# Performance work log

Hardware: AMD Instinct MI355X
Metric: run time of the kernel (lower is better)

## Reference

```python
import jax, jax.numpy as jnp
import numpy as np

# ---- static problem configuration (mirrors Barrier_Net param) ----
B, NN, NO, SD = 100000, 16, 8, 4        # agents, neighbors, obstacles, state dim
H, PHI_OUT, ADIM = 64, 16, 2            # MLP hidden, deepset latent, action dim
DS, B_GAMMA, B_EXPH = 0.2, 0.01, 1.0    # r_safe, barrier gain, barrier exponent
PHI_MIN, PHI_MAX = -1.0, 1.0            # empty-action range
A_MIN, A_MAX = -2.0, 2.0                # final action range
D_OBS = 1 + (NN + 1) * SD + 2 * NO      # 85


def mlp2(x, w1, b1, w2, b2):
    return jax.nn.relu(x @ w1 + b1) @ w2 + b2


def setup_inputs() -> dict:
    key = jax.random.key(0)
    ks = jax.random.split(key, 10)
    x = jax.random.normal(ks[0], (B, D_OBS), jnp.float32)
    x = x.at[:, 0].set(float(NN))  # first entry encodes the neighbor count

    def w(k, shape):
        return jax.random.normal(k, shape, jnp.float32) * 0.1

    return {
        "x": x,
        "phi_w1": w(ks[1], (SD, H)), "phi_b1": jnp.zeros((H,), jnp.float32),
        "phi_w2": w(ks[2], (H, PHI_OUT)), "phi_b2": jnp.zeros((PHI_OUT,), jnp.float32),
        "obs_w1": w(ks[3], (2, H)), "obs_b1": jnp.zeros((H,), jnp.float32),
        "obs_w2": w(ks[4], (H, PHI_OUT)), "obs_b2": jnp.zeros((PHI_OUT,), jnp.float32),
        "rho_w1": w(ks[5], (PHI_OUT, H)), "rho_b1": jnp.zeros((H,), jnp.float32),
        "rho_w2": w(ks[6], (H, ADIM)), "rho_b2": jnp.zeros((ADIM,), jnp.float32),
        "psi_w1": w(ks[7], (ADIM + 2, H)), "psi_b1": jnp.zeros((H,), jnp.float32),
        "psi_w2": w(ks[8], (H, ADIM)), "psi_b2": jnp.zeros((ADIM,), jnp.float32),
    }


def reference(x, phi_w1, phi_b1, phi_w2, phi_b2, obs_w1, obs_b1, obs_w2, obs_b2,
              rho_w1, rho_b1, rho_w2, rho_b2, psi_w1, psi_b1, psi_w2, psi_b2):
    # observation layout: [nn, self(SD), nn relative neighbor states(SD each), no obstacles(2 each)]
    nb = x[:, 1 + SD:1 + SD + NN * SD].reshape(B, NN, SD)   # relative neighbor states
    ob = x[:, 1 + (NN + 1) * SD:].reshape(B, NO, 2)          # relative obstacle positions

    # --- DeepSet: permutation-invariant sum of phi over elements, then rho ---
    phi_sum = mlp2(nb, phi_w1, phi_b1, phi_w2, phi_b2).sum(axis=1)   # [B, PHI_OUT]
    obs_sum = mlp2(ob, obs_w1, obs_b1, obs_w2, obs_b2).sum(axis=1)   # [B, PHI_OUT]
    rho = mlp2(phi_sum + obs_sum, rho_w1, rho_b1, rho_w2, rho_b2)    # [B, ADIM]

    # --- empty(): psi head on cat(rho, g) with tanh range squash to [phi_min, phi_max] ---
    g = x[:, 0:2]
    e = mlp2(jnp.concatenate([rho, g], axis=1), psi_w1, psi_b1, psi_w2, psi_b2)
    empty = (jnp.tanh(e) + 1.0) * 0.5 * (PHI_MAX - PHI_MIN) + PHI_MIN

    # --- barrier: gather neighbor rel-positions, scalar potential, scatter-add per agent ---
    p_ij = -nb[..., 0:2]                                    # [B, NN, 2], p^i - p^j
    h_ij = jnp.linalg.norm(p_ij, axis=-1) - DS              # [B, NN]
    barrier = jnp.sum((B_GAMMA / h_ij ** B_EXPH)[..., None] * p_ij, axis=1)  # [B, 2]

    action = jnp.tanh(empty + barrier)
    return (action + 1.0) * 0.5 * (A_MAX - A_MIN) + A_MIN
```

## Files before the change

kernel.cpp:

```cpp
#include <hip/hip_runtime.h>

#define BATCH 100000

__device__ __forceinline__ float relu(float v) { return fmaxf(v, 0.f); }

__global__ __launch_bounds__(256, 4) void barrier_net(
    const float* __restrict__ x,
    const float* __restrict__ phi_w1, const float* __restrict__ phi_b1,
    const float* __restrict__ phi_w2, const float* __restrict__ phi_b2,
    const float* __restrict__ obs_w1, const float* __restrict__ obs_b1,
    const float* __restrict__ obs_w2, const float* __restrict__ obs_b2,
    const float* __restrict__ rho_w1, const float* __restrict__ rho_b1,
    const float* __restrict__ rho_w2, const float* __restrict__ rho_b2,
    const float* __restrict__ psi_w1, const float* __restrict__ psi_b1,
    const float* __restrict__ psi_w2, const float* __restrict__ psi_b2,
    float2* __restrict__ out)
{
    const int s = blockIdx.x * 256 + threadIdx.x;
    if (s >= BATCH) return;
    const float* xr = x + (size_t)s * 85;

    float g0 = xr[0];
    float g1 = xr[1];
    float nb[16][4];
#pragma unroll
    for (int n = 0; n < 16; ++n)
#pragma unroll
        for (int k = 0; k < 4; ++k)
            nb[n][k] = xr[5 + n * 4 + k];

    float bar0 = 0.f, bar1 = 0.f;
#pragma unroll
    for (int n = 0; n < 16; ++n) {
        float p0 = -nb[n][0], p1 = -nb[n][1];
        float r  = __builtin_amdgcn_sqrtf(fmaf(p0, p0, p1 * p1));
        float sc = 0.01f * __builtin_amdgcn_rcpf(r - 0.2f);
        bar0 = fmaf(sc, p0, bar0);
        bar1 = fmaf(sc, p1, bar1);
    }

    float acc[16];
#pragma unroll
    for (int j = 0; j < 16; ++j)
        acc[j] = fmaf(16.f, phi_b2[j], 8.f * obs_b2[j]);

#pragma unroll 2
    for (int h = 0; h < 64; ++h) {
        float w0 = phi_w1[h], w1 = phi_w1[64 + h], w2 = phi_w1[128 + h], w3 = phi_w1[192 + h];
        float b  = phi_b1[h];
        float hs = 0.f;
#pragma unroll
        for (int n = 0; n < 16; ++n) {
            float t = fmaf(nb[n][0], w0, fmaf(nb[n][1], w1, fmaf(nb[n][2], w2, fmaf(nb[n][3], w3, b))));
            hs += relu(t);
        }
#pragma unroll
        for (int j = 0; j < 16; ++j)
            acc[j] = fmaf(hs, phi_w2[h * 16 + j], acc[j]);
    }

    float obv[8][2];
#pragma unroll
    for (int o = 0; o < 8; ++o) {
        obv[o][0] = xr[69 + o * 2];
        obv[o][1] = xr[69 + o * 2 + 1];
    }
#pragma unroll 2
    for (int h = 0; h < 64; ++h) {
        float w0 = obs_w1[h], w1 = obs_w1[64 + h];
        float b  = obs_b1[h];
        float hs = 0.f;
#pragma unroll
        for (int o = 0; o < 8; ++o)
            hs += relu(fmaf(obv[o][0], w0, fmaf(obv[o][1], w1, b)));
#pragma unroll
        for (int j = 0; j < 16; ++j)
            acc[j] = fmaf(hs, obs_w2[h * 16 + j], acc[j]);
    }

    float r0 = rho_b2[0], r1 = rho_b2[1];
#pragma unroll 2
    for (int h = 0; h < 64; ++h) {
        float t = rho_b1[h];
#pragma unroll
        for (int j = 0; j < 16; ++j)
            t = fmaf(acc[j], rho_w1[j * 64 + h], t);
        t = relu(t);
        r0 = fmaf(t, rho_w2[2 * h],     r0);
        r1 = fmaf(t, rho_w2[2 * h + 1], r1);
    }

    float e0 = psi_b2[0], e1 = psi_b2[1];
#pragma unroll 2
    for (int h = 0; h < 64; ++h) {
        float t = fmaf(r0, psi_w1[h],
                  fmaf(r1, psi_w1[64 + h],
                  fmaf(g0, psi_w1[128 + h],
                  fmaf(g1, psi_w1[192 + h], psi_b1[h]))));
        t = relu(t);
        e0 = fmaf(t, psi_w2[2 * h],     e0);
        e1 = fmaf(t, psi_w2[2 * h + 1], e1);
    }

    float a0 = tanhf(tanhf(e0) + bar0);
    float a1 = tanhf(tanhf(e1) + bar1);
    out[s] = make_float2(2.f * a0, 2.f * a1);
}

extern "C" void kernel_launch(void* const* d_in, const int* in_sizes, int n_in,
                              void* d_out, int out_size, void* d_ws, size_t ws_size,
                              hipStream_t stream) {
    dim3 grid((BATCH + 255) / 256), block(256);
    barrier_net<<<grid, block, 0, stream>>>(
        (const float*)d_in[0],
        (const float*)d_in[1],  (const float*)d_in[2],  (const float*)d_in[3],  (const float*)d_in[4],
        (const float*)d_in[5],  (const float*)d_in[6],  (const float*)d_in[7],  (const float*)d_in[8],
        (const float*)d_in[9],  (const float*)d_in[10], (const float*)d_in[11], (const float*)d_in[12],
        (const float*)d_in[13], (const float*)d_in[14], (const float*)d_in[15], (const float*)d_in[16],
        (float2*)d_out);
}
```

Measured before the change: 154.2 us.

## Split each agent across four lanes with shuffle reductions

Each agent is now handled by four consecutive threads. Each lane processes 4 neighbors and 2 obstacles and a quarter of the rho and psi hidden units, and partial sums are combined with xor shuffles. This raises parallelism and cuts the per-thread register footprint, which allows higher occupancy (launch bounds raised to 8). In exchange it adds shuffle overhead, and every lane still recomputes the full 16-wide phi and obs output accumulation from its partial hidden sums.

```diff
diff --git a/kernel.cpp b/kernel.cpp
--- a/kernel.cpp
+++ b/kernel.cpp
@@ -4,7 +4,7 @@
 
 __device__ __forceinline__ float relu(float v) { return fmaxf(v, 0.f); }
 
-__global__ __launch_bounds__(256, 4) void barrier_net(
+__global__ __launch_bounds__(256, 8) void barrier_net(
     const float* __restrict__ x,
     const float* __restrict__ phi_w1, const float* __restrict__ phi_b1,
     const float* __restrict__ phi_w2, const float* __restrict__ phi_b2,
@@ -16,22 +16,30 @@
     const float* __restrict__ psi_w2, const float* __restrict__ psi_b2,
     float2* __restrict__ out)
 {
-    const int s = blockIdx.x * 256 + threadIdx.x;
+    const int tid = blockIdx.x * 256 + threadIdx.x;
+    const int s = tid >> 2;
+    const int t = tid & 3;
     if (s >= BATCH) return;
     const float* xr = x + (size_t)s * 85;
 
-    float g0 = xr[0];
-    float g1 = xr[1];
-    float nb[16][4];
+    float nb[4][4];
+    const int nbase = 5 + 16 * t;
 #pragma unroll
-    for (int n = 0; n < 16; ++n)
+    for (int n = 0; n < 4; ++n)
 #pragma unroll
         for (int k = 0; k < 4; ++k)
-            nb[n][k] = xr[5 + n * 4 + k];
+            nb[n][k] = xr[nbase + 4 * n + k];
+
+    float ob[2][2];
+    const int obase = 69 + 4 * t;
+    ob[0][0] = xr[obase];     ob[0][1] = xr[obase + 1];
+    ob[1][0] = xr[obase + 2]; ob[1][1] = xr[obase + 3];
+
+    const float g0 = xr[0], g1 = xr[1];
 
     float bar0 = 0.f, bar1 = 0.f;
 #pragma unroll
-    for (int n = 0; n < 16; ++n) {
+    for (int n = 0; n < 4; ++n) {
         float p0 = -nb[n][0], p1 = -nb[n][1];
         float r  = __builtin_amdgcn_sqrtf(fmaf(p0, p0, p1 * p1));
         float sc = 0.01f * __builtin_amdgcn_rcpf(r - 0.2f);
@@ -42,75 +50,94 @@
     float acc[16];
 #pragma unroll
     for (int j = 0; j < 16; ++j)
-        acc[j] = fmaf(16.f, phi_b2[j], 8.f * obs_b2[j]);
+        acc[j] = fmaf(4.f, phi_b2[j], 2.f * obs_b2[j]);
 
-#pragma unroll 2
+#pragma unroll 4
     for (int h = 0; h < 64; ++h) {
         float w0 = phi_w1[h], w1 = phi_w1[64 + h], w2 = phi_w1[128 + h], w3 = phi_w1[192 + h];
         float b  = phi_b1[h];
-        float hs = 0.f;
-#pragma unroll
-        for (int n = 0; n < 16; ++n) {
-            float t = fmaf(nb[n][0], w0, fmaf(nb[n][1], w1, fmaf(nb[n][2], w2, fmaf(nb[n][3], w3, b))));
-            hs += relu(t);
-        }
+        float hs = relu(fmaf(nb[0][0], w0, fmaf(nb[0][1], w1, fmaf(nb[0][2], w2, fmaf(nb[0][3], w3, b)))))
+                 + relu(fmaf(nb[1][0], w0, fmaf(nb[1][1], w1, fmaf(nb[1][2], w2, fmaf(nb[1][3], w3, b)))))
+                 + relu(fmaf(nb[2][0], w0, fmaf(nb[2][1], w1, fmaf(nb[2][2], w2, fmaf(nb[2][3], w3, b)))))
+                 + relu(fmaf(nb[3][0], w0, fmaf(nb[3][1], w1, fmaf(nb[3][2], w2, fmaf(nb[3][3], w3, b)))));
 #pragma unroll
         for (int j = 0; j < 16; ++j)
             acc[j] = fmaf(hs, phi_w2[h * 16 + j], acc[j]);
     }
 
-    float obv[8][2];
-#pragma unroll
-    for (int o = 0; o < 8; ++o) {
-        obv[o][0] = xr[69 + o * 2];
-        obv[o][1] = xr[69 + o * 2 + 1];
-    }
-#pragma unroll 2
+#pragma unroll 4
     for (int h = 0; h < 64; ++h) {
         float w0 = obs_w1[h], w1 = obs_w1[64 + h];
         float b  = obs_b1[h];
-        float hs = 0.f;
-#pragma unroll
-        for (int o = 0; o < 8; ++o)
-            hs += relu(fmaf(obv[o][0], w0, fmaf(obv[o][1], w1, b)));
+        float hs = relu(fmaf(ob[0][0], w0, fmaf(ob[0][1], w1, b)))
+                 + relu(fmaf(ob[1][0], w0, fmaf(ob[1][1], w1, b)));
 #pragma unroll
         for (int j = 0; j < 16; ++j)
             acc[j] = fmaf(hs, obs_w2[h * 16 + j], acc[j]);
     }
 
-    float r0 = rho_b2[0], r1 = rho_b2[1];
+#pragma unroll
+    for (int j = 0; j < 16; ++j) {
+        acc[j] += __shfl_xor(acc[j], 1);
+        acc[j] += __shfl_xor(acc[j], 2);
+    }
+    bar0 += __shfl_xor(bar0, 1); bar0 += __shfl_xor(bar0, 2);
+    bar1 += __shfl_xor(bar1, 1); bar1 += __shfl_xor(bar1, 2);
+
+    float r0 = 0.f, r1 = 0.f;
+    {
+        const float* rw1 = rho_w1 + 16 * t;
+        const float* rw2 = rho_w2 + 32 * t;
+        const float* rb1 = rho_b1 + 16 * t;
 #pragma unroll 2
-    for (int h = 0; h < 64; ++h) {
-        float t = rho_b1[h];
+        for (int i = 0; i < 16; ++i) {
+            float tt = rb1[i];
 #pragma unroll
-        for (int j = 0; j < 16; ++j)
-            t = fmaf(acc[j], rho_w1[j * 64 + h], t);
-        t = relu(t);
-        r0 = fmaf(t, rho_w2[2 * h],     r0);
-        r1 = fmaf(t, rho_w2[2 * h + 1], r1);
+            for (int j = 0; j < 16; ++j)
+                tt = fmaf(acc[j], rw1[j * 64 + i], tt);
+            tt = relu(tt);
+            r0 = fmaf(tt, rw2[2 * i],     r0);
+            r1 = fmaf(tt, rw2[2 * i + 1], r1);
+        }
     }
+    r0 += __shfl_xor(r0, 1); r0 += __shfl_xor(r0, 2);
+    r1 += __shfl_xor(r1, 1); r1 += __shfl_xor(r1, 2);
+    r0 += rho_b2[0];
+    r1 += rho_b2[1];
 
-    float e0 = psi_b2[0], e1 = psi_b2[1];
+    float e0 = 0.f, e1 = 0.f;
+    {
+        const float* pw1 = psi_w1 + 16 * t;
+        const float* pw2 = psi_w2 + 32 * t;
+        const float* pb1 = psi_b1 + 16 * t;
 #pragma unroll 2
-    for (int h = 0; h < 64; ++h) {
-        float t = fmaf(r0, psi_w1[h],
-                  fmaf(r1, psi_w1[64 + h],
-                  fmaf(g0, psi_w1[128 + h],
-                  fmaf(g1, psi_w1[192 + h], psi_b1[h]))));
-        t = relu(t);
-        e0 = fmaf(t, psi_w2[2 * h],     e0);
-        e1 = fmaf(t, psi_w2[2 * h + 1], e1);
+        for (int i = 0; i < 16; ++i) {
+            float tt = fmaf(r0, pw1[i],
+                       fmaf(r1, pw1[64 + i],
+                       fmaf(g0, pw1[128 + i],
+                       fmaf(g1, pw1[192 + i], pb1[i]))));
+            tt = relu(tt);
+            e0 = fmaf(tt, pw2[2 * i],     e0);
+            e1 = fmaf(tt, pw2[2 * i + 1], e1);
+        }
     }
+    e0 += __shfl_xor(e0, 1); e0 += __shfl_xor(e0, 2);
+    e1 += __shfl_xor(e1, 1); e1 += __shfl_xor(e1, 2);
+    e0 += psi_b2[0];
+    e1 += psi_b2[1];
 
-    float a0 = tanhf(tanhf(e0) + bar0);
-    float a1 = tanhf(tanhf(e1) + bar1);
-    out[s] = make_float2(2.f * a0, 2.f * a1);
+    if (t == 0) {
+        float a0 = tanhf(tanhf(e0) + bar0);
+        float a1 = tanhf(tanhf(e1) + bar1);
+        out[s] = make_float2(2.f * a0, 2.f * a1);
+    }
 }
 
 extern "C" void kernel_launch(void* const* d_in, const int* in_sizes, int n_in,
                               void* d_out, int out_size, void* d_ws, size_t ws_size,
                               hipStream_t stream) {
-    dim3 grid((BATCH + 255) / 256), block(256);
+    const int threads = BATCH * 4;
+    dim3 grid((threads + 255) / 256), block(256);
     barrier_net<<<grid, block, 0, stream>>>(
         (const float*)d_in[0],
         (const float*)d_in[1],  (const float*)d_in[2],  (const float*)d_in[3],  (const float*)d_in[4],
```

After: 230.1 us. +49.2%, slower.
